# Kernel tuning notes

Hardware: AMD Instinct MI355X
Metric: run time of the kernel (lower is better)

The kernel has to match this reference:

```python
import jax, jax.numpy as jnp
import numpy as np


def setup_inputs() -> dict:
    key = jax.random.key(0)
    ks = jax.random.split(key, 5)
    B, N, H, S, D = 1, 256, 4, 256, 32
    q = jax.random.normal(ks[0], (B, N, H, S, D), dtype=jnp.float32)
    k = jax.random.normal(ks[1], (B, N, H, S, D), dtype=jnp.float32)
    v = jax.random.normal(ks[2], (B, N, H, S, D), dtype=jnp.float32)
    mask_bias = jax.random.normal(ks[3], (B, N, 1, 1, S), dtype=jnp.float32)
    triangle_bias = jax.random.normal(ks[4], (B, 1, H, S, S), dtype=jnp.float32)
    return {"q": q, "k": k, "v": v, "mask_bias": mask_bias, "triangle_bias": triangle_bias}


def reference(q, k, v, mask_bias, triangle_bias):
    # q,k,v: [B, N, H, S, D]; mask_bias: [B, N, 1, 1, S]; triangle_bias: [B, 1, H, S, S]
    D = q.shape[-1]
    sm_scale = 1.0 / jnp.sqrt(jnp.asarray(D, dtype=q.dtype))
    # scores: [B, N, H, S, S] (query index s attends over key index t)
    scores = jnp.einsum("bnhsd,bnhtd->bnhst", q, k) * sm_scale
    scores = scores + mask_bias + triangle_bias  # broadcast add of both biases
    p = jax.nn.softmax(scores, axis=-1)
    out = jnp.einsum("bnhst,bnhtd->bnhsd", p, v)
    return out
```

## Files before the change

### kernel.cpp

```cpp
#include <hip/hip_runtime.h>

typedef __bf16 bf16;
typedef bf16 bf16x8 __attribute__((ext_vector_type(8)));
typedef bf16 bf16x4 __attribute__((ext_vector_type(4)));
typedef float f32x4 __attribute__((ext_vector_type(4)));

#define SEQ 256
#define DH  32
#define VT_PAD 264
#define P_PAD  40

__global__ __launch_bounds__(256, 4) void attn_mfma_kernel(
    const float* __restrict__ q,
    const float* __restrict__ k,
    const float* __restrict__ v,
    const float* __restrict__ mask_bias,
    const float* __restrict__ tri_bias,
    float* __restrict__ out)
{
    __shared__ bf16 Vt[DH][VT_PAD];
    __shared__ bf16 Pb[4][64][P_PAD];

    const int tid  = threadIdx.x;
    const int wave = tid >> 6;
    const int lane = tid & 63;
    const int l15  = lane & 15;
    const int quad = lane >> 4;

    const int inst = blockIdx.x;
    const int n    = inst >> 2;
    const int h    = inst & 3;

    const float* qb = q + (size_t)inst * SEQ * DH;
    const float* kb = k + (size_t)inst * SEQ * DH;
    const float* vb = v + (size_t)inst * SEQ * DH;
    const float* mb = mask_bias + (size_t)n * SEQ;
    const float* tb = tri_bias + (size_t)h * SEQ * SEQ;

    const float K1    = 0.17677669529663687f * 1.44269504088896f;
    const float LOG2E = 1.44269504088896f;

    #pragma unroll
    for (int i = 0; i < 8; ++i) {
        int idx = i * 256 + tid;
        int t = idx >> 3;
        int d = (idx & 7) * 4;
        float4 tv = ((const float4*)vb)[idx];
        Vt[d + 0][t] = (bf16)tv.x;
        Vt[d + 1][t] = (bf16)tv.y;
        Vt[d + 2][t] = (bf16)tv.z;
        Vt[d + 3][t] = (bf16)tv.w;
    }
    __syncthreads();

    const int s_base = wave * 64;
    bf16x8 qfrag[4];
    #pragma unroll
    for (int st = 0; st < 4; ++st) {
        const float* p = qb + (size_t)(s_base + st * 16 + l15) * DH + quad * 8;
        float4 a = ((const float4*)p)[0];
        float4 b = ((const float4*)p)[1];
        bf16x8 f;
        f[0] = (bf16)a.x; f[1] = (bf16)a.y; f[2] = (bf16)a.z; f[3] = (bf16)a.w;
        f[4] = (bf16)b.x; f[5] = (bf16)b.y; f[6] = (bf16)b.z; f[7] = (bf16)b.w;
        qfrag[st] = f;
    }

    f32x4 oacc[4][2];
    #pragma unroll
    for (int st = 0; st < 4; ++st)
        #pragma unroll
        for (int dt = 0; dt < 2; ++dt)
            oacc[st][dt] = (f32x4){0.f, 0.f, 0.f, 0.f};
    float lpart[4] = {0.f, 0.f, 0.f, 0.f};

    const f32x4 zero4 = {0.f, 0.f, 0.f, 0.f};

    for (int c = 0; c < 8; ++c) {
        #pragma unroll
        for (int half = 0; half < 2; ++half) {
            const int mt = c * 2 + half;
            const int t0 = mt * 16;

            const float* kp = kb + (size_t)(t0 + l15) * DH + quad * 8;
            float4 ka = ((const float4*)kp)[0];
            float4 kc = ((const float4*)kp)[1];
            bf16x8 kfrag;
            kfrag[0] = (bf16)ka.x; kfrag[1] = (bf16)ka.y;
            kfrag[2] = (bf16)ka.z; kfrag[3] = (bf16)ka.w;
            kfrag[4] = (bf16)kc.x; kfrag[5] = (bf16)kc.y;
            kfrag[6] = (bf16)kc.z; kfrag[7] = (bf16)kc.w;

            float4 mk = *(const float4*)(mb + t0 + quad * 4);
            float4 tr[4];
            #pragma unroll
            for (int st = 0; st < 4; ++st) {
                const float* tp = tb + (size_t)(s_base + st * 16 + l15) * SEQ + t0 + quad * 4;
                tr[st] = *(const float4*)tp;
            }
            float mkl0 = mk.x * LOG2E, mkl1 = mk.y * LOG2E;
            float mkl2 = mk.z * LOG2E, mkl3 = mk.w * LOG2E;

            f32x4 cf[4];
            #pragma unroll
            for (int st = 0; st < 4; ++st)
                cf[st] = __builtin_amdgcn_mfma_f32_16x16x32_bf16(kfrag, qfrag[st], zero4, 0, 0, 0);

            #pragma unroll
            for (int st = 0; st < 4; ++st) {
                float p0 = __builtin_amdgcn_exp2f(fmaf(tr[st].x, LOG2E, fmaf(cf[st][0], K1, mkl0)));
                float p1 = __builtin_amdgcn_exp2f(fmaf(tr[st].y, LOG2E, fmaf(cf[st][1], K1, mkl1)));
                float p2 = __builtin_amdgcn_exp2f(fmaf(tr[st].z, LOG2E, fmaf(cf[st][2], K1, mkl2)));
                float p3 = __builtin_amdgcn_exp2f(fmaf(tr[st].w, LOG2E, fmaf(cf[st][3], K1, mkl3)));
                lpart[st] += (p0 + p1) + (p2 + p3);
                bf16x4 pk;
                pk[0] = (bf16)p0; pk[1] = (bf16)p1; pk[2] = (bf16)p2; pk[3] = (bf16)p3;
                *(bf16x4*)&Pb[wave][st * 16 + l15][half * 16 + quad * 4] = pk;
            }
        }

        bf16x8 vf[2];
        #pragma unroll
        for (int dt = 0; dt < 2; ++dt)
            vf[dt] = *(const bf16x8*)&Vt[dt * 16 + l15][c * 32 + quad * 8];
        #pragma unroll
        for (int st = 0; st < 4; ++st) {
            bf16x8 pf = *(const bf16x8*)&Pb[wave][st * 16 + l15][quad * 8];
            #pragma unroll
            for (int dt = 0; dt < 2; ++dt)
                oacc[st][dt] = __builtin_amdgcn_mfma_f32_16x16x32_bf16(pf, vf[dt], oacc[st][dt], 0, 0, 0);
        }
    }

    float linv[4];
    #pragma unroll
    for (int st = 0; st < 4; ++st) {
        float x = lpart[st];
        x += __shfl_xor(x, 16);
        x += __shfl_xor(x, 32);
        linv[st] = 1.0f / x;
    }

    float* ob = out + (size_t)inst * SEQ * DH;
    #pragma unroll
    for (int st = 0; st < 4; ++st) {
        #pragma unroll
        for (int r = 0; r < 4; ++r) {
            float invr = __shfl(linv[st], quad * 4 + r);
            int s = s_base + st * 16 + quad * 4 + r;
            float* orow = ob + (size_t)s * DH;
            orow[l15]      = oacc[st][0][r] * invr;
            orow[16 + l15] = oacc[st][1][r] * invr;
        }
    }
}

extern "C" void kernel_launch(void* const* d_in, const int* in_sizes, int n_in,
                              void* d_out, int out_size, void* d_ws, size_t ws_size,
                              hipStream_t stream) {
    const float* q    = (const float*)d_in[0];
    const float* k    = (const float*)d_in[1];
    const float* v    = (const float*)d_in[2];
    const float* mask = (const float*)d_in[3];
    const float* tri  = (const float*)d_in[4];
    float* out = (float*)d_out;

    attn_mfma_kernel<<<dim3(256 * 4), dim3(256), 0, stream>>>(q, k, v, mask, tri, out);
}
```

Measured before the change: 180.6 us.

## Switch to 32x32x16 MFMA with in-register P via permlane32 swap

Moves the QK^T and PV products from 16x16x32 to 32x32x16 bf16 MFMA tiles. The probability matrix is repacked in registers with permlane32_swap so it no longer round-trips through LDS. K is staged as bf16 in shared memory once per block, and the mask bias is pre-scaled into shared memory. Triangle-bias loads are software-prefetched one chunk ahead. This cuts redundant global K loads and LDS P traffic, at the cost of more registers per thread, which may reduce occupancy.

```diff
diff --git a/kernel.cpp b/kernel.cpp
--- a/kernel.cpp
+++ b/kernel.cpp
@@ -1,14 +1,22 @@
 #include <hip/hip_runtime.h>
 
 typedef __bf16 bf16;
+typedef bf16 bf16x2 __attribute__((ext_vector_type(2)));
+typedef bf16 bf16x4 __attribute__((ext_vector_type(4)));
 typedef bf16 bf16x8 __attribute__((ext_vector_type(8)));
-typedef bf16 bf16x4 __attribute__((ext_vector_type(4)));
 typedef float f32x4 __attribute__((ext_vector_type(4)));
+typedef float f32x16 __attribute__((ext_vector_type(16)));
+typedef int i32x2 __attribute__((ext_vector_type(2)));
 
 #define SEQ 256
 #define DH  32
 #define VT_PAD 264
-#define P_PAD  40
+#define KB_PAD 40
+
+static __device__ __forceinline__ int pk2(float a, float b) {
+    bf16x2 t; t[0] = (bf16)a; t[1] = (bf16)b;
+    int r; __builtin_memcpy(&r, &t, sizeof(r)); return r;
+}
 
 __global__ __launch_bounds__(256, 4) void attn_mfma_kernel(
     const float* __restrict__ q,
@@ -19,13 +27,14 @@
     float* __restrict__ out)
 {
     __shared__ bf16 Vt[DH][VT_PAD];
-    __shared__ bf16 Pb[4][64][P_PAD];
+    __shared__ bf16 Kb[SEQ][KB_PAD];
+    __shared__ float Ml[SEQ];
 
     const int tid  = threadIdx.x;
     const int wave = tid >> 6;
     const int lane = tid & 63;
-    const int l15  = lane & 15;
-    const int quad = lane >> 4;
+    const int l31  = lane & 31;
+    const int hi   = lane >> 5;
 
     const int inst = blockIdx.x;
     const int n    = inst >> 2;
@@ -40,118 +49,143 @@
     const float K1    = 0.17677669529663687f * 1.44269504088896f;
     const float LOG2E = 1.44269504088896f;
 
+    const int sbase = wave * 64;
+
+    const float* trow0 = tb + (size_t)(sbase + l31) * SEQ + 4 * hi;
+    const float* trow1 = trow0 + 32 * SEQ;
+
+    f32x4 tpre0[4];
+    #pragma unroll
+    for (int g = 0; g < 4; ++g)
+        tpre0[g] = *(const f32x4*)(trow0 + 8 * g);
+
+    bf16x8 qf[2][2];
+    #pragma unroll
+    for (int st = 0; st < 2; ++st)
+        #pragma unroll
+        for (int dh = 0; dh < 2; ++dh) {
+            const float* p = qb + (size_t)(sbase + st * 32 + l31) * DH + dh * 16 + hi * 8;
+            f32x4 a = ((const f32x4*)p)[0];
+            f32x4 b = ((const f32x4*)p)[1];
+            bf16x8 f;
+            f[0]=(bf16)a[0]; f[1]=(bf16)a[1]; f[2]=(bf16)a[2]; f[3]=(bf16)a[3];
+            f[4]=(bf16)b[0]; f[5]=(bf16)b[1]; f[6]=(bf16)b[2]; f[7]=(bf16)b[3];
+            qf[st][dh] = f;
+        }
+
     #pragma unroll
     for (int i = 0; i < 8; ++i) {
         int idx = i * 256 + tid;
-        int t = idx >> 3;
-        int d = (idx & 7) * 4;
-        float4 tv = ((const float4*)vb)[idx];
-        Vt[d + 0][t] = (bf16)tv.x;
-        Vt[d + 1][t] = (bf16)tv.y;
-        Vt[d + 2][t] = (bf16)tv.z;
-        Vt[d + 3][t] = (bf16)tv.w;
+        int t   = idx >> 3;
+        int d4  = (idx & 7) * 4;
+        f32x4 tv = ((const f32x4*)vb)[idx];
+        Vt[d4 + 0][t] = (bf16)tv[0];
+        Vt[d4 + 1][t] = (bf16)tv[1];
+        Vt[d4 + 2][t] = (bf16)tv[2];
+        Vt[d4 + 3][t] = (bf16)tv[3];
+        f32x4 tk = ((const f32x4*)kb)[idx];
+        bf16x4 kk;
+        kk[0]=(bf16)tk[0]; kk[1]=(bf16)tk[1]; kk[2]=(bf16)tk[2]; kk[3]=(bf16)tk[3];
+        *(bf16x4*)&Kb[t][d4] = kk;
     }
+    Ml[tid] = mb[tid] * LOG2E;
     __syncthreads();
 
-    const int s_base = wave * 64;
-    bf16x8 qfrag[4];
-    #pragma unroll
-    for (int st = 0; st < 4; ++st) {
-        const float* p = qb + (size_t)(s_base + st * 16 + l15) * DH + quad * 8;
-        float4 a = ((const float4*)p)[0];
-        float4 b = ((const float4*)p)[1];
-        bf16x8 f;
-        f[0] = (bf16)a.x; f[1] = (bf16)a.y; f[2] = (bf16)a.z; f[3] = (bf16)a.w;
-        f[4] = (bf16)b.x; f[5] = (bf16)b.y; f[6] = (bf16)b.z; f[7] = (bf16)b.w;
-        qfrag[st] = f;
+    f32x16 oacc0 = {}, oacc1 = {};
+    float lp0 = 0.f, lp1 = 0.f;
+    const f32x16 z16 = {};
+
+    #pragma unroll
+    for (int c = 0; c < 8; ++c) {
+        const int tb0 = c * 32;
+
+        f32x4 t1g[4];
+        #pragma unroll
+        for (int g = 0; g < 4; ++g)
+            t1g[g] = *(const f32x4*)(trow1 + tb0 + 8 * g);
+
+        bf16x8 kf0 = *(const bf16x8*)&Kb[tb0 + l31][hi * 8];
+        bf16x8 kf1 = *(const bf16x8*)&Kb[tb0 + l31][16 + hi * 8];
+
+        f32x4 mkv[4];
+        #pragma unroll
+        for (int g = 0; g < 4; ++g)
+            mkv[g] = *(const f32x4*)&Ml[tb0 + 8 * g + 4 * hi];
+
+        f32x16 cf = __builtin_amdgcn_mfma_f32_32x32x16_bf16(kf0, qf[0][0], z16, 0, 0, 0);
+        cf = __builtin_amdgcn_mfma_f32_32x32x16_bf16(kf1, qf[0][1], cf, 0, 0, 0);
+
+        int A[8];
+        #pragma unroll
+        for (int g = 0; g < 4; ++g) {
+            float p0 = __builtin_amdgcn_exp2f(fmaf(cf[4*g+0], K1, fmaf(tpre0[g][0], LOG2E, mkv[g][0])));
+            float p1 = __builtin_amdgcn_exp2f(fmaf(cf[4*g+1], K1, fmaf(tpre0[g][1], LOG2E, mkv[g][1])));
+            float p2 = __builtin_amdgcn_exp2f(fmaf(cf[4*g+2], K1, fmaf(tpre0[g][2], LOG2E, mkv[g][2])));
+            float p3 = __builtin_amdgcn_exp2f(fmaf(cf[4*g+3], K1, fmaf(tpre0[g][3], LOG2E, mkv[g][3])));
+            lp0 += (p0 + p1) + (p2 + p3);
+            A[2*g]   = pk2(p0, p1);
+            A[2*g+1] = pk2(p2, p3);
+        }
+
+        if (c < 7) {
+            #pragma unroll
+            for (int g = 0; g < 4; ++g)
+                tpre0[g] = *(const f32x4*)(trow0 + tb0 + 32 + 8 * g);
+        }
+
+        i32x2 s0 = __builtin_amdgcn_permlane32_swap(A[0], A[2], false, false);
+        i32x2 s1 = __builtin_amdgcn_permlane32_swap(A[1], A[3], false, false);
+        i32x2 s2 = __builtin_amdgcn_permlane32_swap(A[4], A[6], false, false);
+        i32x2 s3 = __builtin_amdgcn_permlane32_swap(A[5], A[7], false, false);
+        union { int i[4]; bf16x8 v; } pa0, pa1;
+        pa0.i[0] = s0[0]; pa0.i[1] = s1[0]; pa0.i[2] = s0[1]; pa0.i[3] = s1[1];
+        pa1.i[0] = s2[0]; pa1.i[1] = s3[0]; pa1.i[2] = s2[1]; pa1.i[3] = s3[1];
+
+        bf16x8 vf0 = *(const bf16x8*)&Vt[l31][tb0 + hi * 8];
+        bf16x8 vf1 = *(const bf16x8*)&Vt[l31][tb0 + 16 + hi * 8];
+
+        oacc0 = __builtin_amdgcn_mfma_f32_32x32x16_bf16(pa0.v, vf0, oacc0, 0, 0, 0);
+        oacc0 = __builtin_amdgcn_mfma_f32_32x32x16_bf16(pa1.v, vf1, oacc0, 0, 0, 0);
+
+        cf = __builtin_amdgcn_mfma_f32_32x32x16_bf16(kf0, qf[1][0], z16, 0, 0, 0);
+        cf = __builtin_amdgcn_mfma_f32_32x32x16_bf16(kf1, qf[1][1], cf, 0, 0, 0);
+
+        #pragma unroll
+        for (int g = 0; g < 4; ++g) {
+            float p0 = __builtin_amdgcn_exp2f(fmaf(cf[4*g+0], K1, fmaf(t1g[g][0], LOG2E, mkv[g][0])));
+            float p1 = __builtin_amdgcn_exp2f(fmaf(cf[4*g+1], K1, fmaf(t1g[g][1], LOG2E, mkv[g][1])));
+            float p2 = __builtin_amdgcn_exp2f(fmaf(cf[4*g+2], K1, fmaf(t1g[g][2], LOG2E, mkv[g][2])));
+            float p3 = __builtin_amdgcn_exp2f(fmaf(cf[4*g+3], K1, fmaf(t1g[g][3], LOG2E, mkv[g][3])));
+            lp1 += (p0 + p1) + (p2 + p3);
+            A[2*g]   = pk2(p0, p1);
+            A[2*g+1] = pk2(p2, p3);
+        }
+
+        s0 = __builtin_amdgcn_permlane32_swap(A[0], A[2], false, false);
+        s1 = __builtin_amdgcn_permlane32_swap(A[1], A[3], false, false);
+        s2 = __builtin_amdgcn_permlane32_swap(A[4], A[6], false, false);
+        s3 = __builtin_amdgcn_permlane32_swap(A[5], A[7], false, false);
+        union { int i[4]; bf16x8 v; } pb0, pb1;
+        pb0.i[0] = s0[0]; pb0.i[1] = s1[0]; pb0.i[2] = s0[1]; pb0.i[3] = s1[1];
+        pb1.i[0] = s2[0]; pb1.i[1] = s3[0]; pb1.i[2] = s2[1]; pb1.i[3] = s3[1];
+
+        oacc1 = __builtin_amdgcn_mfma_f32_32x32x16_bf16(pb0.v, vf0, oacc1, 0, 0, 0);
+        oacc1 = __builtin_amdgcn_mfma_f32_32x32x16_bf16(pb1.v, vf1, oacc1, 0, 0, 0);
     }
 
-    f32x4 oacc[4][2];
-    #pragma unroll
-    for (int st = 0; st < 4; ++st)
-        #pragma unroll
-        for (int dt = 0; dt < 2; ++dt)
-            oacc[st][dt] = (f32x4){0.f, 0.f, 0.f, 0.f};
-    float lpart[4] = {0.f, 0.f, 0.f, 0.f};
-
-    const f32x4 zero4 = {0.f, 0.f, 0.f, 0.f};
-
-    for (int c = 0; c < 8; ++c) {
-        #pragma unroll
-        for (int half = 0; half < 2; ++half) {
-            const int mt = c * 2 + half;
-            const int t0 = mt * 16;
-
-            const float* kp = kb + (size_t)(t0 + l15) * DH + quad * 8;
-            float4 ka = ((const float4*)kp)[0];
-            float4 kc = ((const float4*)kp)[1];
-            bf16x8 kfrag;
-            kfrag[0] = (bf16)ka.x; kfrag[1] = (bf16)ka.y;
-            kfrag[2] = (bf16)ka.z; kfrag[3] = (bf16)ka.w;
-            kfrag[4] = (bf16)kc.x; kfrag[5] = (bf16)kc.y;
-            kfrag[6] = (bf16)kc.z; kfrag[7] = (bf16)kc.w;
-
-            float4 mk = *(const float4*)(mb + t0 + quad * 4);
-            float4 tr[4];
-            #pragma unroll
-            for (int st = 0; st < 4; ++st) {
-                const float* tp = tb + (size_t)(s_base + st * 16 + l15) * SEQ + t0 + quad * 4;
-                tr[st] = *(const float4*)tp;
-            }
-            float mkl0 = mk.x * LOG2E, mkl1 = mk.y * LOG2E;
-            float mkl2 = mk.z * LOG2E, mkl3 = mk.w * LOG2E;
-
-            f32x4 cf[4];
-            #pragma unroll
-            for (int st = 0; st < 4; ++st)
-                cf[st] = __builtin_amdgcn_mfma_f32_16x16x32_bf16(kfrag, qfrag[st], zero4, 0, 0, 0);
-
-            #pragma unroll
-            for (int st = 0; st < 4; ++st) {
-                float p0 = __builtin_amdgcn_exp2f(fmaf(tr[st].x, LOG2E, fmaf(cf[st][0], K1, mkl0)));
-                float p1 = __builtin_amdgcn_exp2f(fmaf(tr[st].y, LOG2E, fmaf(cf[st][1], K1, mkl1)));
-                float p2 = __builtin_amdgcn_exp2f(fmaf(tr[st].z, LOG2E, fmaf(cf[st][2], K1, mkl2)));
-                float p3 = __builtin_amdgcn_exp2f(fmaf(tr[st].w, LOG2E, fmaf(cf[st][3], K1, mkl3)));
-                lpart[st] += (p0 + p1) + (p2 + p3);
-                bf16x4 pk;
-                pk[0] = (bf16)p0; pk[1] = (bf16)p1; pk[2] = (bf16)p2; pk[3] = (bf16)p3;
-                *(bf16x4*)&Pb[wave][st * 16 + l15][half * 16 + quad * 4] = pk;
-            }
-        }
-
-        bf16x8 vf[2];
-        #pragma unroll
-        for (int dt = 0; dt < 2; ++dt)
-            vf[dt] = *(const bf16x8*)&Vt[dt * 16 + l15][c * 32 + quad * 8];
-        #pragma unroll
-        for (int st = 0; st < 4; ++st) {
-            bf16x8 pf = *(const bf16x8*)&Pb[wave][st * 16 + l15][quad * 8];
-            #pragma unroll
-            for (int dt = 0; dt < 2; ++dt)
-                oacc[st][dt] = __builtin_amdgcn_mfma_f32_16x16x32_bf16(pf, vf[dt], oacc[st][dt], 0, 0, 0);
-        }
-    }
-
-    float linv[4];
-    #pragma unroll
-    for (int st = 0; st < 4; ++st) {
-        float x = lpart[st];
-        x += __shfl_xor(x, 16);
-        x += __shfl_xor(x, 32);
-        linv[st] = 1.0f / x;
-    }
+    lp0 += __shfl_xor(lp0, 32);
+    lp1 += __shfl_xor(lp1, 32);
+    const float li0 = 1.0f / lp0;
+    const float li1 = 1.0f / lp1;
 
     float* ob = out + (size_t)inst * SEQ * DH;
     #pragma unroll
-    for (int st = 0; st < 4; ++st) {
-        #pragma unroll
-        for (int r = 0; r < 4; ++r) {
-            float invr = __shfl(linv[st], quad * 4 + r);
-            int s = s_base + st * 16 + quad * 4 + r;
-            float* orow = ob + (size_t)s * DH;
-            orow[l15]      = oacc[st][0][r] * invr;
-            orow[16 + l15] = oacc[st][1][r] * invr;
-        }
+    for (int r = 0; r < 16; ++r) {
+        const int srow = (r & 3) + 8 * (r >> 2) + 4 * hi;
+        float i0 = __shfl(li0, srow);
+        float i1 = __shfl(li1, srow);
+        ob[(size_t)(sbase + srow) * DH + l31]      = oacc0[r] * i0;
+        ob[(size_t)(sbase + 32 + srow) * DH + l31] = oacc1[r] * i1;
     }
 }
 
```

Measured after the change: 401.9 us. 123% more time.
